# Kernel tuning notes

Hardware: AMD Instinct MI355X
Metric: run time of the kernel (lower is better)

## Reference

```python
import jax, jax.numpy as jnp
import numpy as np

NUM_HEADS = 12


def setup_inputs() -> dict:
    key = jax.random.key(0)
    ks = jax.random.split(key, 10)
    B, N, C = 8, 1024, 768
    H = NUM_HEADS
    return {
        "x": jax.random.normal(ks[0], (B, N, C), dtype=jnp.float32),
        "geometric": jax.random.uniform(ks[1], (B, 1, 1, 1), dtype=jnp.float32),
        "text": jax.random.uniform(ks[2], (B, 1, 1, 1), dtype=jnp.float32),
        "color": jax.random.uniform(ks[3], (B, 1, 1, 1), dtype=jnp.float32),
        "W_qkv": jax.random.normal(ks[4], (C, 3 * C), dtype=jnp.float32) * 0.02,
        "W_proj": jax.random.normal(ks[5], (C, C), dtype=jnp.float32) * 0.02,
        "b_proj": jax.random.normal(ks[6], (C,), dtype=jnp.float32) * 0.02,
        "geo_bias": jax.random.normal(ks[7], (1, H, 1, 1), dtype=jnp.float32) * 0.1,
        "txt_bias": jax.random.normal(ks[8], (1, H, 1, 1), dtype=jnp.float32) * 0.1,
        "col_bias": jax.random.normal(ks[9], (1, H, 1, 1), dtype=jnp.float32) * 0.1,
    }


def reference(x, geometric, text, color, W_qkv, W_proj, b_proj, geo_bias, txt_bias, col_bias):
    B, N, C = x.shape
    H = NUM_HEADS
    Dh = C // H
    scale = Dh ** -0.5
    # qkv: [B, N, 3, H, Dh] -> q,k,v each [B, H, N, Dh]
    qkv = (x @ W_qkv).reshape(B, N, 3, H, Dh)
    q = jnp.transpose(qkv[:, :, 0], (0, 2, 1, 3))
    k = jnp.transpose(qkv[:, :, 1], (0, 2, 1, 3))
    v = jnp.transpose(qkv[:, :, 2], (0, 2, 1, 3))
    # scores [B, H, N, N] with additive per-head logo biases
    attn = jnp.einsum("bhnd,bhmd->bhnm", q, k) * scale
    attn = attn + geo_bias * geometric + txt_bias * text + col_bias * color
    attn = jax.nn.softmax(attn, axis=-1)
    out = jnp.einsum("bhnm,bhmd->bhnd", attn, v)  # [B, H, N, Dh]
    out = jnp.transpose(out, (0, 2, 1, 3)).reshape(B, N, C)
    return out @ W_proj + b_proj
```

## Files before the change

### kernel.cpp

```cpp
#include <hip/hip_runtime.h>
#include <hip/hip_bf16.h>


typedef __bf16 b16x8 __attribute__((ext_vector_type(8)));
typedef float f32x4 __attribute__((ext_vector_type(4)));

__device__ __forceinline__ ushort f2b(float f) {
    union { float f; uint u; } v; v.f = f;
    uint u = v.u;
    u += 0x7fffu + ((u >> 16) & 1u);
    return (ushort)(u >> 16);
}

__device__ __forceinline__ uint packbf(float a, float b) {
    union { float f; uint u; } ua, ub; ua.f = a; ub.f = b;
    return ((ua.u + 0x8000u) >> 16) | ((ub.u + 0x8000u) & 0xffff0000u);
}

__device__ __forceinline__ void async_cp16(const void* g, void* l) {
    __builtin_amdgcn_global_load_lds(
        (const __attribute__((address_space(1))) unsigned int*)g,
        (__attribute__((address_space(3))) unsigned int*)l, 16, 0, 0);
}


__global__ __launch_bounds__(256)
void k_prep(const float* __restrict__ x, ushort* __restrict__ xb,
            const float* __restrict__ Wqkv, ushort* __restrict__ wqkvt,
            const float* __restrict__ Wproj, ushort* __restrict__ wprojt) {
    __shared__ ushort T[64][65];
    const int blk = blockIdx.x;
    const int t   = threadIdx.x;

    if (blk < 6144) {
        const int i = blk * 256 + t;
        const float4 v = reinterpret_cast<const float4*>(x)[i];
        ushort4 o;
        o.x = f2b(v.x); o.y = f2b(v.y); o.z = f2b(v.z); o.w = f2b(v.w);
        reinterpret_cast<ushort4*>(xb)[i] = o;
        return;
    }

    const bool isqkv = (blk < 6576);
    const int idx = isqkv ? (blk - 6144) : (blk - 6576);
    const int Nin = isqkv ? 2304 : 768;
    const float* W  = isqkv ? Wqkv : Wproj;
    ushort* Wt      = isqkv ? wqkvt : wprojt;
    const int k0 = (idx % 12) * 64;
    const int n0 = (idx / 12) * 64;
    const int r  = t >> 4, cg = (t & 15) * 4;
    #pragma unroll
    for (int rr = 0; rr < 64; rr += 16) {
        const float4 v = *reinterpret_cast<const float4*>(&W[(size_t)(k0 + r + rr) * Nin + n0 + cg]);
        T[r + rr][cg + 0] = f2b(v.x); T[r + rr][cg + 1] = f2b(v.y);
        T[r + rr][cg + 2] = f2b(v.z); T[r + rr][cg + 3] = f2b(v.w);
    }
    __syncthreads();
    #pragma unroll
    for (int rr = 0; rr < 64; rr += 16) {
        ushort4 o;
        o.x = T[cg + 0][r + rr]; o.y = T[cg + 1][r + rr];
        o.z = T[cg + 2][r + rr]; o.w = T[cg + 3][r + rr];
        *reinterpret_cast<ushort4*>(&Wt[(size_t)(n0 + r + rr) * 768 + k0 + cg]) = o;
    }
}


template<int MODE>
__global__ __launch_bounds__(256, 2)
void k_gemm(const ushort* __restrict__ A, const ushort* __restrict__ Bt,
            ushort* __restrict__ qo, ushort* __restrict__ ko, ushort* __restrict__ vo,
            float* __restrict__ co, const float* __restrict__ bias,
            int M, int N, int K) {
    __shared__ ushort As[128 * 32];
    __shared__ ushort Bs[128 * 32];
    const int tid  = threadIdx.x;
    const int lane = tid & 63;
    const int w    = tid >> 6;
    const int wm   = w >> 1, wn = w & 1;
    const int m16  = lane & 15, quad = lane >> 4;
    const int mbase = blockIdx.y * 128, nbase = blockIdx.x * 128;

    f32x4 acc[4][4];
    #pragma unroll
    for (int i = 0; i < 4; i++)
        #pragma unroll
        for (int j = 0; j < 4; j++) acc[i][j] = (f32x4){0.f, 0.f, 0.f, 0.f};

    const int rS = w * 32 + (lane >> 2);
    const int cS = (lane & 3) * 8;
    ushort* ldsA0 = &As[(w * 2 + 0) * 512];
    ushort* ldsA1 = &As[(w * 2 + 1) * 512];
    ushort* ldsB0 = &Bs[(w * 2 + 0) * 512];
    ushort* ldsB1 = &Bs[(w * 2 + 1) * 512];
    const ushort* gA0 = &A [(size_t)(mbase + rS)      * K + cS];
    const ushort* gA1 = &A [(size_t)(mbase + rS + 16) * K + cS];
    const ushort* gB0 = &Bt[(size_t)(nbase + rS)      * K + cS];
    const ushort* gB1 = &Bt[(size_t)(nbase + rS + 16) * K + cS];

    for (int kt = 0; kt < K; kt += 32) {
        __syncthreads();
        async_cp16(gA0 + kt, ldsA0);
        async_cp16(gA1 + kt, ldsA1);
        async_cp16(gB0 + kt, ldsB0);
        async_cp16(gB1 + kt, ldsB1);
        __syncthreads();

        b16x8 af[4], bf[4];
        #pragma unroll
        for (int i = 0; i < 4; i++)
            af[i] = *reinterpret_cast<const b16x8*>(&As[(wm * 64 + i * 16 + m16) * 32 + quad * 8]);
        #pragma unroll
        for (int j = 0; j < 4; j++)
            bf[j] = *reinterpret_cast<const b16x8*>(&Bs[(wn * 64 + j * 16 + m16) * 32 + quad * 8]);
        #pragma unroll
        for (int i = 0; i < 4; i++)
            #pragma unroll
            for (int j = 0; j < 4; j++)
                acc[i][j] = __builtin_amdgcn_mfma_f32_16x16x32_bf16(bf[j], af[i], acc[i][j], 0, 0, 0);
    }

    #pragma unroll
    for (int j = 0; j < 4; j++) {
        const int f0 = nbase + wn * 64 + j * 16 + quad * 4;
        #pragma unroll
        for (int i = 0; i < 4; i++) {
            const int tok = mbase + wm * 64 + i * 16 + m16;
            const int b = tok >> 10, n = tok & 1023;
            if (MODE == 0) {
                const int s   = f0 / 768;
                const int rem = f0 - s * 768;
                const int h   = rem >> 6;
                const int d0  = rem & 63;
                if (s < 2) {
                    ushort4 pk;
                    pk.x = f2b(acc[i][j][0]); pk.y = f2b(acc[i][j][1]);
                    pk.z = f2b(acc[i][j][2]); pk.w = f2b(acc[i][j][3]);
                    ushort* base = (s == 0) ? qo : ko;
                    *reinterpret_cast<ushort4*>(
                        &base[((size_t)(b * 12 + h) * 1024 + n) * 64 + d0]) = pk;
                } else {
                    #pragma unroll
                    for (int r = 0; r < 4; r++)
                        vo[((size_t)(b * 12 + h) * 64 + d0 + r) * 1024 + n] =
                            f2b(acc[i][j][r]);
                }
            } else {
                float4 val;
                val.x = acc[i][j][0] + bias[f0 + 0];
                val.y = acc[i][j][1] + bias[f0 + 1];
                val.z = acc[i][j][2] + bias[f0 + 2];
                val.w = acc[i][j][3] + bias[f0 + 3];
                *reinterpret_cast<float4*>(&co[(size_t)tok * N + f0]) = val;
            }
        }
    }
}


#define AP 72

__global__ __launch_bounds__(256)
void k_attn(const ushort* __restrict__ qa, const ushort* __restrict__ ka,
            const ushort* __restrict__ vt, ushort* __restrict__ ao) {
    __shared__ ushort Ks[64 * AP];
    __shared__ ushort Vs[64 * AP];

    const int l    = blockIdx.x;
    const int xcd  = l & 7;
    const int g    = l >> 3;
    const int head = (g % 12) * 8 + xcd;
    const int qsup = g / 12;
    const int tid  = threadIdx.x;
    const int w    = tid >> 6;
    const int lane = tid & 63;
    const int n    = lane & 15;
    const int q    = lane >> 4;

    const ushort* qh = qa + (size_t)head * 65536;
    const ushort* kh = ka + (size_t)head * 65536;
    const ushort* vh = vt + (size_t)head * 65536;
    const int qrow0 = qsup * 128 + w * 32;

    b16x8 bq0[2], bq1[2];
    #pragma unroll
    for (int u = 0; u < 2; u++) {
        bq0[u] = *reinterpret_cast<const b16x8*>(&qh[(qrow0 + u * 16 + n) * 64 + q * 8]);
        bq1[u] = *reinterpret_cast<const b16x8*>(&qh[(qrow0 + u * 16 + n) * 64 + 32 + q * 8]);
    }

    const int kr0 = tid >> 3, kc0 = (tid & 7) * 8;
    const int kr1 = kr0 + 32, kc1 = kc0;

    int4 kg0, kg1, vg0, vg1;
    kg0 = *reinterpret_cast<const int4*>(&kh[(0 + kr0) * 64 + kc0]);
    kg1 = *reinterpret_cast<const int4*>(&kh[(0 + kr1) * 64 + kc1]);
    vg0 = *reinterpret_cast<const int4*>(&vh[kr0 * 1024 + 0 + kc0]);
    vg1 = *reinterpret_cast<const int4*>(&vh[kr1 * 1024 + 0 + kc1]);

    f32x4 o[2][4];
    #pragma unroll
    for (int u = 0; u < 2; u++)
        #pragma unroll
        for (int dt = 0; dt < 4; dt++) o[u][dt] = (f32x4){0, 0, 0, 0};
    float Lacc[2] = {0.f, 0.f};

    const float SC = 0.125f * 1.4426950408889634f;
    const int s0 = ((q & 1) * 2) * 16 + n;
    const int s1 = s0 + 16;
    const bool lowq = (q < 2);

    for (int m0 = 0; m0 < 1024; m0 += 64) {
        *reinterpret_cast<int4*>(&Ks[kr0 * AP + kc0]) = kg0;
        *reinterpret_cast<int4*>(&Ks[kr1 * AP + kc1]) = kg1;
        *reinterpret_cast<int4*>(&Vs[kr0 * AP + kc0]) = vg0;
        *reinterpret_cast<int4*>(&Vs[kr1 * AP + kc1]) = vg1;
        __syncthreads();

        if (m0 + 64 < 1024) {
            kg0 = *reinterpret_cast<const int4*>(&kh[(m0 + 64 + kr0) * 64 + kc0]);
            kg1 = *reinterpret_cast<const int4*>(&kh[(m0 + 64 + kr1) * 64 + kc1]);
            vg0 = *reinterpret_cast<const int4*>(&vh[kr0 * 1024 + m0 + 64 + kc0]);
            vg1 = *reinterpret_cast<const int4*>(&vh[kr1 * 1024 + m0 + 64 + kc1]);
        }

        #pragma unroll
        for (int mc = 0; mc < 2; mc++) {
            b16x8 ka0t[2], ka1t[2];
            #pragma unroll
            for (int t = 0; t < 2; t++) {
                ka0t[t] = *reinterpret_cast<const b16x8*>(&Ks[(mc * 32 + t * 16 + n) * AP + q * 8]);
                ka1t[t] = *reinterpret_cast<const b16x8*>(&Ks[(mc * 32 + t * 16 + n) * AP + 32 + q * 8]);
            }
            f32x4 st[2][2];
            #pragma unroll
            for (int u = 0; u < 2; u++)
                #pragma unroll
                for (int t = 0; t < 2; t++) {
                    st[u][t] = (f32x4){0, 0, 0, 0};
                    st[u][t] = __builtin_amdgcn_mfma_f32_16x16x32_bf16(ka0t[t], bq0[u], st[u][t], 0, 0, 0);
                    st[u][t] = __builtin_amdgcn_mfma_f32_16x16x32_bf16(ka1t[t], bq1[u], st[u][t], 0, 0, 0);
                }

            union { uint4 u4; b16x8 v; } bp[2];
            #pragma unroll
            for (int u = 0; u < 2; u++) {
                float p00 = __builtin_amdgcn_exp2f(st[u][0][0] * SC);
                float p01 = __builtin_amdgcn_exp2f(st[u][0][1] * SC);
                float p02 = __builtin_amdgcn_exp2f(st[u][0][2] * SC);
                float p03 = __builtin_amdgcn_exp2f(st[u][0][3] * SC);
                float p10 = __builtin_amdgcn_exp2f(st[u][1][0] * SC);
                float p11 = __builtin_amdgcn_exp2f(st[u][1][1] * SC);
                float p12 = __builtin_amdgcn_exp2f(st[u][1][2] * SC);
                float p13 = __builtin_amdgcn_exp2f(st[u][1][3] * SC);
                Lacc[u] += ((p00 + p01) + (p02 + p03)) + ((p10 + p11) + (p12 + p13));

                const uint pk00 = packbf(p00, p01), pk01 = packbf(p02, p03);
                const uint pk10 = packbf(p10, p11), pk11 = packbf(p12, p13);

                uint a, b, dw0, dw1, dw2, dw3;
                a = __shfl((int)pk00, s0); b = __shfl((int)pk10, s0); dw0 = lowq ? a : b;
                a = __shfl((int)pk01, s0); b = __shfl((int)pk11, s0); dw1 = lowq ? a : b;
                a = __shfl((int)pk00, s1); b = __shfl((int)pk10, s1); dw2 = lowq ? a : b;
                a = __shfl((int)pk01, s1); b = __shfl((int)pk11, s1); dw3 = lowq ? a : b;
                bp[u].u4 = (uint4){dw0, dw1, dw2, dw3};
            }

            #pragma unroll
            for (int dt = 0; dt < 4; dt++) {
                const b16x8 av = *reinterpret_cast<const b16x8*>(
                    &Vs[(dt * 16 + n) * AP + mc * 32 + q * 8]);
                #pragma unroll
                for (int u = 0; u < 2; u++)
                    o[u][dt] = __builtin_amdgcn_mfma_f32_16x16x32_bf16(av, bp[u].v, o[u][dt], 0, 0, 0);
            }
        }
        __syncthreads();
    }

    const int bb = head / 12, h = head - bb * 12;
    #pragma unroll
    for (int u = 0; u < 2; u++) {
        float L = Lacc[u];
        L += __shfl_xor(L, 16);
        L += __shfl_xor(L, 32);
        const float inv = 1.f / L;
        ushort* dst = ao + ((size_t)(bb * 1024 + qrow0 + u * 16 + n)) * 768 + h * 64 + q * 4;
        #pragma unroll
        for (int dt = 0; dt < 4; dt++) {
            ushort4 pk;
            pk.x = f2b(o[u][dt][0] * inv);
            pk.y = f2b(o[u][dt][1] * inv);
            pk.z = f2b(o[u][dt][2] * inv);
            pk.w = f2b(o[u][dt][3] * inv);
            *reinterpret_cast<ushort4*>(dst + dt * 16) = pk;
        }
    }
}


extern "C" void kernel_launch(void* const* d_in, const int* in_sizes, int n_in,
                              void* d_out, int out_size, void* d_ws, size_t ws_size,
                              hipStream_t stream) {
    (void)in_sizes; (void)n_in; (void)out_size; (void)ws_size;
    const float* x     = (const float*)d_in[0];
    const float* Wqkv  = (const float*)d_in[4];
    const float* Wproj = (const float*)d_in[5];
    const float* bproj = (const float*)d_in[6];
    float* out = (float*)d_out;

    char* ws = (char*)d_ws;
    ushort* xb     = (ushort*)ws; ws += (size_t)8192 * 768 * 2;
    ushort* wqkvt  = (ushort*)ws; ws += (size_t)2304 * 768 * 2;
    ushort* wprojt = (ushort*)ws; ws += (size_t)768  * 768 * 2;
    ushort* qa     = (ushort*)ws; ws += (size_t)96 * 1024 * 64 * 2;
    ushort* ka     = (ushort*)ws; ws += (size_t)96 * 1024 * 64 * 2;
    ushort* vt     = (ushort*)ws; ws += (size_t)96 * 64 * 1024 * 2;
    ushort* ao     = (ushort*)ws; ws += (size_t)8192 * 768 * 2;

    k_prep<<<dim3(6720), dim3(256), 0, stream>>>(x, xb, Wqkv, wqkvt, Wproj, wprojt);
    k_gemm<0><<<dim3(18, 64), dim3(256), 0, stream>>>(xb, wqkvt, qa, ka, vt,
                                                      nullptr, nullptr, 8192, 2304, 768);
    k_attn<<<dim3(768), dim3(256), 0, stream>>>(qa, ka, vt, ao);
    k_gemm<1><<<dim3(6, 64), dim3(256), 0, stream>>>(ao, wprojt, nullptr, nullptr, nullptr,
                                                     out, bproj, 8192, 768, 768);
}
```

Before: 217.6 us.

## Double-buffer GEMM LDS tiles and remap blocks across XCDs

The GEMM kernel now keeps two LDS buffers for its A and B tiles. It prefetches the next K-slice with async global-to-LDS copies while MFMAs run on the current slice, and drops one barrier per iteration. The grid is flattened to 1D and remapped so consecutive block IDs assigned to the same XCD share M-rows, to improve L2 reuse. This doubles LDS per block, which may limit occupancy, and it relies on the barrier's implicit wait for the async loads to finish.

Result: no change. 214.8 us (-1.3%).

```diff
diff --git a/kernel.cpp b/kernel.cpp
--- a/kernel.cpp
+++ b/kernel.cpp
@@ -72,14 +72,19 @@
             ushort* __restrict__ qo, ushort* __restrict__ ko, ushort* __restrict__ vo,
             float* __restrict__ co, const float* __restrict__ bias,
             int M, int N, int K) {
-    __shared__ ushort As[128 * 32];
-    __shared__ ushort Bs[128 * 32];
+    __shared__ ushort As[2][128 * 32];
+    __shared__ ushort Bs[2][128 * 32];
+    const int id   = blockIdx.x;
+    const int xcd  = id & 7;
+    const int s    = id >> 3;
+    const int by   = xcd * 8 + (s & 7);
+    const int bx   = s >> 3;
     const int tid  = threadIdx.x;
     const int lane = tid & 63;
     const int w    = tid >> 6;
     const int wm   = w >> 1, wn = w & 1;
     const int m16  = lane & 15, quad = lane >> 4;
-    const int mbase = blockIdx.y * 128, nbase = blockIdx.x * 128;
+    const int mbase = by * 128, nbase = bx * 128;
 
     f32x4 acc[4][4];
     #pragma unroll
@@ -89,30 +94,35 @@
 
     const int rS = w * 32 + (lane >> 2);
     const int cS = (lane & 3) * 8;
-    ushort* ldsA0 = &As[(w * 2 + 0) * 512];
-    ushort* ldsA1 = &As[(w * 2 + 1) * 512];
-    ushort* ldsB0 = &Bs[(w * 2 + 0) * 512];
-    ushort* ldsB1 = &Bs[(w * 2 + 1) * 512];
+    const int wOff0 = (w * 2 + 0) * 512;
+    const int wOff1 = (w * 2 + 1) * 512;
     const ushort* gA0 = &A [(size_t)(mbase + rS)      * K + cS];
     const ushort* gA1 = &A [(size_t)(mbase + rS + 16) * K + cS];
     const ushort* gB0 = &Bt[(size_t)(nbase + rS)      * K + cS];
     const ushort* gB1 = &Bt[(size_t)(nbase + rS + 16) * K + cS];
 
+    async_cp16(gA0, &As[0][wOff0]);
+    async_cp16(gA1, &As[0][wOff1]);
+    async_cp16(gB0, &Bs[0][wOff0]);
+    async_cp16(gB1, &Bs[0][wOff1]);
+
     for (int kt = 0; kt < K; kt += 32) {
+        const int cur = (kt >> 5) & 1, nxt = cur ^ 1;
         __syncthreads();
-        async_cp16(gA0 + kt, ldsA0);
-        async_cp16(gA1 + kt, ldsA1);
-        async_cp16(gB0 + kt, ldsB0);
-        async_cp16(gB1 + kt, ldsB1);
-        __syncthreads();
+        if (kt + 32 < K) {
+            async_cp16(gA0 + kt + 32, &As[nxt][wOff0]);
+            async_cp16(gA1 + kt + 32, &As[nxt][wOff1]);
+            async_cp16(gB0 + kt + 32, &Bs[nxt][wOff0]);
+            async_cp16(gB1 + kt + 32, &Bs[nxt][wOff1]);
+        }
 
         b16x8 af[4], bf[4];
         #pragma unroll
         for (int i = 0; i < 4; i++)
-            af[i] = *reinterpret_cast<const b16x8*>(&As[(wm * 64 + i * 16 + m16) * 32 + quad * 8]);
+            af[i] = *reinterpret_cast<const b16x8*>(&As[cur][(wm * 64 + i * 16 + m16) * 32 + quad * 8]);
         #pragma unroll
         for (int j = 0; j < 4; j++)
-            bf[j] = *reinterpret_cast<const b16x8*>(&Bs[(wn * 64 + j * 16 + m16) * 32 + quad * 8]);
+            bf[j] = *reinterpret_cast<const b16x8*>(&Bs[cur][(wn * 64 + j * 16 + m16) * 32 + quad * 8]);
         #pragma unroll
         for (int i = 0; i < 4; i++)
             #pragma unroll
@@ -128,15 +138,15 @@
             const int tok = mbase + wm * 64 + i * 16 + m16;
             const int b = tok >> 10, n = tok & 1023;
             if (MODE == 0) {
-                const int s   = f0 / 768;
-                const int rem = f0 - s * 768;
+                const int sp  = f0 / 768;
+                const int rem = f0 - sp * 768;
                 const int h   = rem >> 6;
                 const int d0  = rem & 63;
-                if (s < 2) {
+                if (sp < 2) {
                     ushort4 pk;
                     pk.x = f2b(acc[i][j][0]); pk.y = f2b(acc[i][j][1]);
                     pk.z = f2b(acc[i][j][2]); pk.w = f2b(acc[i][j][3]);
-                    ushort* base = (s == 0) ? qo : ko;
+                    ushort* base = (sp == 0) ? qo : ko;
                     *reinterpret_cast<ushort4*>(
                         &base[((size_t)(b * 12 + h) * 1024 + n) * 64 + d0]) = pk;
                 } else {
@@ -319,9 +329,9 @@
     ushort* ao     = (ushort*)ws; ws += (size_t)8192 * 768 * 2;
 
     k_prep<<<dim3(6720), dim3(256), 0, stream>>>(x, xb, Wqkv, wqkvt, Wproj, wprojt);
-    k_gemm<0><<<dim3(18, 64), dim3(256), 0, stream>>>(xb, wqkvt, qa, ka, vt,
-                                                      nullptr, nullptr, 8192, 2304, 768);
+    k_gemm<0><<<dim3(1152), dim3(256), 0, stream>>>(xb, wqkvt, qa, ka, vt,
+                                                    nullptr, nullptr, 8192, 2304, 768);
     k_attn<<<dim3(768), dim3(256), 0, stream>>>(qa, ka, vt, ao);
-    k_gemm<1><<<dim3(6, 64), dim3(256), 0, stream>>>(ao, wprojt, nullptr, nullptr, nullptr,
-                                                     out, bproj, 8192, 768, 768);
-}
+    k_gemm<1><<<dim3(384), dim3(256), 0, stream>>>(ao, wprojt, nullptr, nullptr, nullptr,
+                                                   out, bproj, 8192, 768, 768);
+}
```
